# Kernel optimization log

Measured on AMD Instinct MI355X. Metric: run time of the kernel, lower is better.

Reference implementation:

```python
import jax, jax.numpy as jnp
import numpy as np

B, T, E = 4, 2048, 1024
H = 16
QK_SQUEEZE = 2
S = E // QK_SQUEEZE          # squeeze_dim = 512
SHD = S // H                 # squeeze_head_dim = 32
HD = E // H                  # head_dim = 64
SCALING = SHD ** -0.5


def setup_inputs() -> dict:
    key = jax.random.key(0)
    ks = jax.random.split(key, 9)
    def w(k, shape, fan_in):
        return jax.random.normal(k, shape, jnp.float32) * (fan_in ** -0.5)
    return {
        "hidden_states": jax.random.normal(ks[0], (B, T, E), jnp.float32),
        "Wq": w(ks[1], (E, S), E), "bq": jnp.zeros((S,), jnp.float32),
        "Wk": w(ks[2], (E, S), E), "bk": jnp.zeros((S,), jnp.float32),
        "Wv": w(ks[3], (E, E), E), "bv": jnp.zeros((E,), jnp.float32),
        "Wo": w(ks[4], (E, E), E), "bo": jnp.zeros((E,), jnp.float32),
    }


def reference(hidden_states, Wq, bq, Wk, bk, Wv, bv, Wo, bo):
    # Projections; Q pre-scaled as in the torch module.
    q = ((hidden_states @ Wq + bq) * SCALING).reshape(B, T, H, SHD)
    k = (hidden_states @ Wk + bk).reshape(B, T, H, SHD)
    v = (hidden_states @ Wv + bv).reshape(B, T, H, HD)
    # [B, H, Tq, Tk] attention logits with squeezed head dim.
    attn = jnp.einsum("bqhd,bkhd->bhqk", q, k)
    p = jax.nn.softmax(attn, axis=-1)  # dropout p=0.0 -> identity
    out = jnp.einsum("bhqk,bkhd->bqhd", p, v).reshape(B, T, E)
    return out @ Wo + bo
```

## Files before the change

### kernel.cpp

```cpp
#include <hip/hip_runtime.h>
#include <stdint.h>


#define QSCALE (0.17677669529663687f * 1.4426950408889634f)

typedef __bf16 bf16x8 __attribute__((ext_vector_type(8)));
typedef float f32x4 __attribute__((ext_vector_type(4)));
typedef float f32x8 __attribute__((ext_vector_type(8)));
typedef float f32x16 __attribute__((ext_vector_type(16)));
typedef unsigned int u32x2 __attribute__((ext_vector_type(2)));
typedef unsigned int u32x4v __attribute__((ext_vector_type(4)));

static __device__ __forceinline__ unsigned short f2b(float f) {
  return __builtin_bit_cast(unsigned short, (__bf16)f);
}
static __device__ __forceinline__ unsigned int cvtpk(float lo, float hi) {
  unsigned int r;
  asm("v_cvt_pk_bf16_f32 %0, %1, %2" : "=v"(r) : "v"(lo), "v"(hi));
  return r;
}
static __device__ __forceinline__ void gl_lds16(const void* g, void* s) {
  __builtin_amdgcn_global_load_lds(
      (const __attribute__((address_space(1))) unsigned int*)(uintptr_t)g,
      (__attribute__((address_space(3))) unsigned int*)(uintptr_t)s, 16, 0, 0);
}
static __device__ __forceinline__ void pswap(unsigned int& a, unsigned int& b) {
#if __has_builtin(__builtin_amdgcn_permlane32_swap)
  u32x2 r = __builtin_amdgcn_permlane32_swap(a, b, false, false);
  a = r.x;
  b = r.y;
#else
  asm("v_permlane32_swap_b32 %0, %1" : "+v"(a), "+v"(b));
#endif
}

__global__ void k_cvt_hs(const float* __restrict__ in, unsigned short* __restrict__ out) {
  int i = (blockIdx.x * 256 + threadIdx.x) * 4;
  float4 v = *(const float4*)(in + i);
  ushort4 u = make_ushort4(f2b(v.x), f2b(v.y), f2b(v.z), f2b(v.w));
  *(ushort4*)(out + i) = u;
}

__global__ void k_cvt_wT(const float* __restrict__ W, unsigned short* __restrict__ WT,
                         int N, float scale) {
  __shared__ float tile[64][65];
  const int kt = blockIdx.x & 15;
  const int nt = blockIdx.x >> 4;
  const int k0 = kt * 64, n0 = nt * 64;
  const int t = threadIdx.x;
  {
    int kl = t >> 2, c = t & 3;
    const float* src = W + (size_t)(k0 + kl) * N + n0 + c * 16;
#pragma unroll
    for (int j = 0; j < 4; j++) {
      float4 v = *(const float4*)(src + j * 4);
      tile[kl][c * 16 + j * 4 + 0] = v.x;
      tile[kl][c * 16 + j * 4 + 1] = v.y;
      tile[kl][c * 16 + j * 4 + 2] = v.z;
      tile[kl][c * 16 + j * 4 + 3] = v.w;
    }
  }
  __syncthreads();
  {
    int nl = t >> 2, c2 = t & 3;
    unsigned short us[16];
#pragma unroll
    for (int j = 0; j < 16; j++) us[j] = f2b(tile[c2 * 16 + j][nl] * scale);
    uint4 a, b;
    a.x = (unsigned)us[0] | ((unsigned)us[1] << 16);
    a.y = (unsigned)us[2] | ((unsigned)us[3] << 16);
    a.z = (unsigned)us[4] | ((unsigned)us[5] << 16);
    a.w = (unsigned)us[6] | ((unsigned)us[7] << 16);
    b.x = (unsigned)us[8] | ((unsigned)us[9] << 16);
    b.y = (unsigned)us[10] | ((unsigned)us[11] << 16);
    b.z = (unsigned)us[12] | ((unsigned)us[13] << 16);
    b.w = (unsigned)us[14] | ((unsigned)us[15] << 16);
    unsigned short* dst = WT + (size_t)(n0 + nl) * 1024 + k0 + c2 * 16;
    *(uint4*)dst = a;
    *(uint4*)(dst + 8) = b;
  }
}

__global__ void k_bias(const float* __restrict__ bq, const float* __restrict__ bk,
                       const float* __restrict__ bv, float* __restrict__ bqkv) {
  int n = blockIdx.x * 256 + threadIdx.x;
  float v;
  if (n < 512) v = bq[n] * QSCALE;
  else if (n < 1024) v = bk[n - 512];
  else v = bv[n - 1024];
  bqkv[n] = v;
}

template <int MODE>
__global__ __launch_bounds__(256) void k_gemm(
    const unsigned short* __restrict__ A, const unsigned short* __restrict__ BT,
    const float* __restrict__ bias, int M, int N,
    unsigned short* __restrict__ qo, unsigned short* __restrict__ ko,
    unsigned short* __restrict__ vo, float* __restrict__ fo) {
  constexpr int K = 1024;
  __shared__ alignas(128) char smem[16384];
  const int tid = threadIdx.x;
  const int w = tid >> 6, l = tid & 63, lm = l & 15, lc = l >> 4;
  const int nmt = M >> 7;
  const int mt = blockIdx.x % nmt, nt = blockIdx.x / nmt;
  const int brow = mt << 7, bcol = nt << 7;
  const int wm = w >> 1, wn = w & 1;
  f32x4 acc[4][4] = {};
  const int ca = w * 64 + l;

  for (int k0 = 0; k0 < K; k0 += 32) {
#pragma unroll
    for (int j = 0; j < 2; j++) {
      int c = j * 256 + ca;
      gl_lds16(A + (size_t)(brow + (c >> 2)) * K + k0 + (c & 3) * 8,
               smem + (j * 256 + w * 64) * 16);
      gl_lds16(BT + (size_t)(bcol + (c >> 2)) * K + k0 + (c & 3) * 8,
               smem + 8192 + (j * 256 + w * 64) * 16);
    }
    __syncthreads();
    bf16x8 af[4], bf[4];
#pragma unroll
    for (int i = 0; i < 4; i++) {
      af[i] = *(const bf16x8*)(smem + (wm * 64 + i * 16 + lm) * 64 + lc * 16);
      bf[i] = *(const bf16x8*)(smem + 8192 + (wn * 64 + i * 16 + lm) * 64 + lc * 16);
    }
#pragma unroll
    for (int ai = 0; ai < 4; ai++)
#pragma unroll
      for (int bj = 0; bj < 4; bj++)
        acc[ai][bj] = __builtin_amdgcn_mfma_f32_16x16x32_bf16(af[ai], bf[bj], acc[ai][bj], 0, 0, 0);
    __syncthreads();
  }

#pragma unroll
  for (int bj = 0; bj < 4; bj++) {
    const int n = bcol + wn * 64 + bj * 16 + lm;
    const float bv_ = bias[n];
#pragma unroll
    for (int ai = 0; ai < 4; ai++) {
      const int m0 = brow + wm * 64 + ai * 16 + lc * 4;
      f32x4 v = acc[ai][bj];
      const float x0 = v[0] + bv_, x1 = v[1] + bv_, x2 = v[2] + bv_, x3 = v[3] + bv_;
      if constexpr (MODE == 0) {
        const int b = m0 >> 11, t0 = m0 & 2047;
        if (n < 1024) {
          unsigned short* dst = (n < 512) ? qo : ko;
          const int nn = n & 511, h = nn >> 5, d = nn & 31;
          const size_t base = ((size_t)((b << 4) + h) * 2048 + t0) * 32 + d;
          dst[base + 0 * 32] = f2b(x0);
          dst[base + 1 * 32] = f2b(x1);
          dst[base + 2 * 32] = f2b(x2);
          dst[base + 3 * 32] = f2b(x3);
        } else {
          const int e = n - 1024, h = e >> 6, hd = e & 63;
          ushort4 u = make_ushort4(f2b(x0), f2b(x1), f2b(x2), f2b(x3));
          *(ushort4*)(vo + (((size_t)((b << 4) + h) * 256 + (t0 >> 3)) * 64 + hd) * 8 +
                      (t0 & 7)) = u;
        }
      } else {
        float* dst = fo + (size_t)m0 * N + n;
        dst[0 * N] = x0;
        dst[1 * N] = x1;
        dst[2 * N] = x2;
        dst[3 * N] = x3;
      }
    }
  }
}

__global__ __launch_bounds__(128, 2) void k_attn6(
    const unsigned short* __restrict__ qb, const unsigned short* __restrict__ kb,
    const unsigned short* __restrict__ v3, unsigned short* __restrict__ aout) {
  __shared__ float red[64][67];
  const int tid = threadIdx.x, kvh = tid >> 6, l = tid & 63;
  const int l31 = l & 31, hf = l >> 5;
  const int xcd = blockIdx.x & 7, slot = blockIdx.x >> 3;
  const int bh = xcd + ((slot >> 5) << 3);
  const int qrow0 = (slot & 31) << 6;

  const unsigned short* qrow = qb + ((size_t)bh * 2048 + qrow0 + l31) * 32 + hf * 8;
  const bf16x8 qA0 = *(const bf16x8*)(qrow);
  const bf16x8 qA1 = *(const bf16x8*)(qrow + 16);
  const bf16x8 qB0 = *(const bf16x8*)(qrow + 1024);
  const bf16x8 qB1 = *(const bf16x8*)(qrow + 1024 + 16);

  const unsigned short* kp = kb + ((size_t)bh * 2048 + kvh * 1024 + l31) * 32 + hf * 8;
  const unsigned short* vp = v3 + (((size_t)bh * 256 + kvh * 128 + hf) * 64 + l31) * 8;

  f32x16 oA0 = {}, oA1 = {}, oB0 = {}, oB1 = {};
  f32x4 lsA4 = {}, lsB4 = {};

  auto tile_body = [&](bf16x8 kf0, bf16x8 kf1, bf16x8 va00, bf16x8 va01, bf16x8 va10,
                       bf16x8 va11) {
    f32x16 sA = {}, sB = {};
    sA = __builtin_amdgcn_mfma_f32_32x32x16_bf16(kf0, qA0, sA, 0, 0, 0);
    sA = __builtin_amdgcn_mfma_f32_32x32x16_bf16(kf1, qA1, sA, 0, 0, 0);
    sB = __builtin_amdgcn_mfma_f32_32x32x16_bf16(kf0, qB0, sB, 0, 0, 0);
    sB = __builtin_amdgcn_mfma_f32_32x32x16_bf16(kf1, qB1, sB, 0, 0, 0);

#pragma unroll
    for (int i = 0; i < 16; i++) sA[i] = __builtin_amdgcn_exp2f(sA[i]);
#pragma unroll
    for (int i = 0; i < 16; i++) sB[i] = __builtin_amdgcn_exp2f(sB[i]);
    {
      f32x8 t8 = __builtin_shufflevector(sA, sA, 0, 1, 2, 3, 4, 5, 6, 7) +
                 __builtin_shufflevector(sA, sA, 8, 9, 10, 11, 12, 13, 14, 15);
      lsA4 += __builtin_shufflevector(t8, t8, 0, 1, 2, 3) +
              __builtin_shufflevector(t8, t8, 4, 5, 6, 7);
    }
    {
      f32x8 t8 = __builtin_shufflevector(sB, sB, 0, 1, 2, 3, 4, 5, 6, 7) +
                 __builtin_shufflevector(sB, sB, 8, 9, 10, 11, 12, 13, 14, 15);
      lsB4 += __builtin_shufflevector(t8, t8, 0, 1, 2, 3) +
              __builtin_shufflevector(t8, t8, 4, 5, 6, 7);
    }
    unsigned int pa[8], pb[8];
#pragma unroll
    for (int i = 0; i < 8; i++) pa[i] = cvtpk(sA[2 * i], sA[2 * i + 1]);
#pragma unroll
    for (int i = 0; i < 8; i++) pb[i] = cvtpk(sB[2 * i], sB[2 * i + 1]);
    pswap(pa[0], pa[2]);
    pswap(pa[1], pa[3]);
    pswap(pa[4], pa[6]);
    pswap(pa[5], pa[7]);
    pswap(pb[0], pb[2]);
    pswap(pb[1], pb[3]);
    pswap(pb[4], pb[6]);
    pswap(pb[5], pb[7]);
    const bf16x8 fA0 = __builtin_bit_cast(bf16x8, (u32x4v){pa[0], pa[1], pa[2], pa[3]});
    const bf16x8 fA1 = __builtin_bit_cast(bf16x8, (u32x4v){pa[4], pa[5], pa[6], pa[7]});
    const bf16x8 fB0 = __builtin_bit_cast(bf16x8, (u32x4v){pb[0], pb[1], pb[2], pb[3]});
    const bf16x8 fB1 = __builtin_bit_cast(bf16x8, (u32x4v){pb[4], pb[5], pb[6], pb[7]});

    __builtin_amdgcn_s_setprio(1);
    oA0 = __builtin_amdgcn_mfma_f32_32x32x16_bf16(va00, fA0, oA0, 0, 0, 0);
    oA1 = __builtin_amdgcn_mfma_f32_32x32x16_bf16(va01, fA0, oA1, 0, 0, 0);
    oB0 = __builtin_amdgcn_mfma_f32_32x32x16_bf16(va00, fB0, oB0, 0, 0, 0);
    oB1 = __builtin_amdgcn_mfma_f32_32x32x16_bf16(va01, fB0, oB1, 0, 0, 0);
    oA0 = __builtin_amdgcn_mfma_f32_32x32x16_bf16(va10, fA1, oA0, 0, 0, 0);
    oA1 = __builtin_amdgcn_mfma_f32_32x32x16_bf16(va11, fA1, oA1, 0, 0, 0);
    oB0 = __builtin_amdgcn_mfma_f32_32x32x16_bf16(va10, fB1, oB0, 0, 0, 0);
    oB1 = __builtin_amdgcn_mfma_f32_32x32x16_bf16(va11, fB1, oB1, 0, 0, 0);
    __builtin_amdgcn_s_setprio(0);
  };

  bf16x8 kf0 = *(const bf16x8*)(kp);
  bf16x8 kf1 = *(const bf16x8*)(kp + 16);
  bf16x8 va00 = *(const bf16x8*)(vp + 0);
  bf16x8 va01 = *(const bf16x8*)(vp + 256);
  bf16x8 va10 = *(const bf16x8*)(vp + 1024);
  bf16x8 va11 = *(const bf16x8*)(vp + 1280);

  for (int it = 0; it < 31; ++it) {
    kp += 1024;
    vp += 2048;
    const bf16x8 nk0 = *(const bf16x8*)(kp);
    const bf16x8 nk1 = *(const bf16x8*)(kp + 16);
    const bf16x8 nv00 = *(const bf16x8*)(vp + 0);
    const bf16x8 nv01 = *(const bf16x8*)(vp + 256);
    const bf16x8 nv10 = *(const bf16x8*)(vp + 1024);
    const bf16x8 nv11 = *(const bf16x8*)(vp + 1280);

    tile_body(kf0, kf1, va00, va01, va10, va11);

    kf0 = nk0;
    kf1 = nk1;
    va00 = nv00;
    va01 = nv01;
    va10 = nv10;
    va11 = nv11;
  }
  tile_body(kf0, kf1, va00, va01, va10, va11);

  float lsA = (lsA4[0] + lsA4[1]) + (lsA4[2] + lsA4[3]);
  float lsB = (lsB4[0] + lsB4[1]) + (lsB4[2] + lsB4[3]);
  lsA += __shfl_xor(lsA, 32);
  lsB += __shfl_xor(lsB, 32);

  if (kvh == 1) {
    float* r = &red[l][0];
#pragma unroll
    for (int i = 0; i < 16; i++) {
      r[i] = oA0[i];
      r[16 + i] = oA1[i];
      r[32 + i] = oB0[i];
      r[48 + i] = oB1[i];
    }
    r[64] = lsA;
    r[65] = lsB;
  }
  __syncthreads();
  if (kvh == 0) {
    const float* r = &red[l][0];
#pragma unroll
    for (int i = 0; i < 16; i++) {
      oA0[i] += r[i];
      oA1[i] += r[16 + i];
      oB0[i] += r[32 + i];
      oB1[i] += r[48 + i];
    }
    lsA += r[64];
    lsB += r[65];

    const int b = bh >> 4, hh = bh & 15;
    const float rA = 1.0f / lsA, rB = 1.0f / lsB;
    unsigned short* orowA = aout + ((size_t)(b * 2048 + qrow0 + l31)) * 1024 + hh * 64;
    unsigned short* orowB = orowA + (size_t)32 * 1024;
#pragma unroll
    for (int hc = 0; hc < 2; hc++) {
#pragma unroll
      for (int rg = 0; rg < 4; rg++) {
        const f32x16& oa = hc ? oA1 : oA0;
        ushort4 ua = make_ushort4(f2b(oa[rg * 4 + 0] * rA), f2b(oa[rg * 4 + 1] * rA),
                                  f2b(oa[rg * 4 + 2] * rA), f2b(oa[rg * 4 + 3] * rA));
        *(ushort4*)(orowA + hc * 32 + rg * 8 + hf * 4) = ua;
        const f32x16& ob = hc ? oB1 : oB0;
        ushort4 ub = make_ushort4(f2b(ob[rg * 4 + 0] * rB), f2b(ob[rg * 4 + 1] * rB),
                                  f2b(ob[rg * 4 + 2] * rB), f2b(ob[rg * 4 + 3] * rB));
        *(ushort4*)(orowB + hc * 32 + rg * 8 + hf * 4) = ub;
      }
    }
  }
}

extern "C" void kernel_launch(void* const* d_in, const int* in_sizes, int n_in,
                              void* d_out, int out_size, void* d_ws, size_t ws_size,
                              hipStream_t stream) {
  const float* hs = (const float*)d_in[0];
  const float* Wq = (const float*)d_in[1];
  const float* bq = (const float*)d_in[2];
  const float* Wk = (const float*)d_in[3];
  const float* bk = (const float*)d_in[4];
  const float* Wv = (const float*)d_in[5];
  const float* bv = (const float*)d_in[6];
  const float* Wo = (const float*)d_in[7];
  const float* bo = (const float*)d_in[8];

  char* ws = (char*)d_ws;
  unsigned short* hsb   = (unsigned short*)(ws + 0);
  unsigned short* wqkvT = (unsigned short*)(ws + 16777216);
  unsigned short* woT   = (unsigned short*)(ws + 20971520);
  float*          bqkv  = (float*)        (ws + 23068672);
  unsigned short* qbuf  = (unsigned short*)(ws + 23076864);
  unsigned short* kbuf  = (unsigned short*)(ws + 31465472);
  unsigned short* vTb   = (unsigned short*)(ws + 39854080);
  unsigned short* aoutb = (unsigned short*)(ws + 56631296);

  k_cvt_hs<<<8192, 256, 0, stream>>>(hs, hsb);
  k_cvt_wT<<<128, 256, 0, stream>>>(Wq, wqkvT, 512, QSCALE);
  k_cvt_wT<<<128, 256, 0, stream>>>(Wk, wqkvT + 512 * 1024, 512, 1.0f);
  k_cvt_wT<<<256, 256, 0, stream>>>(Wv, wqkvT + 1024 * 1024, 1024, 1.0f);
  k_cvt_wT<<<256, 256, 0, stream>>>(Wo, woT, 1024, 1.0f);
  k_bias<<<8, 256, 0, stream>>>(bq, bk, bv, bqkv);

  k_gemm<0><<<64 * 16, 256, 0, stream>>>(hsb, wqkvT, bqkv, 8192, 2048,
                                         qbuf, kbuf, vTb, nullptr);
  k_attn6<<<2048, 128, 0, stream>>>(qbuf, kbuf, vTb, aoutb);
  k_gemm<1><<<64 * 8, 256, 0, stream>>>(aoutb, woT, bo, 8192, 1024,
                                        nullptr, nullptr, nullptr, (float*)d_out);
}
```

Baseline: 166.9 us.

## Replace QKV projection GEMM with 256x256-tile double-buffered 512-thread kernel

Adds a dedicated QKV GEMM kernel that uses 256x256 output tiles, 512 threads and 128KB of LDS. The K loop is double-buffered, with direct global-to-LDS loads and MFMA phases run at raised wave priority. Larger tiles raise operand reuse per LDS byte, and the 256-block grid covers the GPU in one wave. In exchange, occupancy drops to one block per CU, and the unswizzled 128-byte LDS rows may cause bank conflicts on fragment reads.

```diff
diff --git a/kernel.cpp b/kernel.cpp
--- a/kernel.cpp
+++ b/kernel.cpp
@@ -89,6 +89,109 @@
   else if (n < 1024) v = bk[n - 512];
   else v = bv[n - 1024];
   bqkv[n] = v;
+}
+
+__global__ __launch_bounds__(512, 2) void k_gemm256qkv(
+    const unsigned short* __restrict__ A, const unsigned short* __restrict__ BT,
+    const float* __restrict__ bias,
+    unsigned short* __restrict__ qo, unsigned short* __restrict__ ko,
+    unsigned short* __restrict__ vo) {
+  __shared__ alignas(128) char smem[131072];
+  const int tid = threadIdx.x;
+  const int w = tid >> 6, l = tid & 63, lm = l & 15, lc = l >> 4;
+  const int wm = w >> 2, wn = w & 3;
+  const int mt = blockIdx.x & 31, nt = blockIdx.x >> 5;
+  const int brow = mt << 8, bcol = nt << 8;
+
+  f32x4 acc[8][4] = {};
+
+  auto stage = [&](int kt, int buf) {
+    const unsigned short* As = A + (size_t)brow * 1024 + kt * 64;
+    const unsigned short* Bs = BT + (size_t)bcol * 1024 + kt * 64;
+    char* la = smem + buf * 32768;
+    char* lb = smem + 65536 + buf * 32768;
+#pragma unroll
+    for (int j = 0; j < 4; j++) {
+      const int p = j * 512 + tid;
+      gl_lds16(As + (size_t)(p >> 3) * 1024 + (p & 7) * 8, la + (j * 512 + w * 64) * 16);
+      gl_lds16(Bs + (size_t)(p >> 3) * 1024 + (p & 7) * 8, lb + (j * 512 + w * 64) * 16);
+    }
+  };
+
+  auto phase = [&](const char* la, const char* lb, int mg, int ng) {
+    bf16x8 af[4][2], bf[2][2];
+#pragma unroll
+    for (int mi = 0; mi < 4; mi++)
+#pragma unroll
+      for (int kk = 0; kk < 2; kk++)
+        af[mi][kk] = *(const bf16x8*)(la + (wm * 128 + (mg + mi) * 16 + lm) * 128 +
+                                      kk * 64 + lc * 16);
+#pragma unroll
+    for (int ni = 0; ni < 2; ni++)
+#pragma unroll
+      for (int kk = 0; kk < 2; kk++)
+        bf[ni][kk] = *(const bf16x8*)(lb + (wn * 64 + (ng + ni) * 16 + lm) * 128 +
+                                      kk * 64 + lc * 16);
+    __builtin_amdgcn_s_setprio(1);
+#pragma unroll
+    for (int mi = 0; mi < 4; mi++)
+#pragma unroll
+      for (int ni = 0; ni < 2; ni++)
+#pragma unroll
+        for (int kk = 0; kk < 2; kk++)
+          acc[mg + mi][ng + ni] = __builtin_amdgcn_mfma_f32_16x16x32_bf16(
+              af[mi][kk], bf[ni][kk], acc[mg + mi][ng + ni], 0, 0, 0);
+    __builtin_amdgcn_s_setprio(0);
+    __builtin_amdgcn_sched_barrier(0);
+  };
+
+  auto ktile = [&](int buf) {
+    const char* la = smem + buf * 32768;
+    const char* lb = smem + 65536 + buf * 32768;
+    phase(la, lb, 0, 0);
+    phase(la, lb, 4, 0);
+    phase(la, lb, 0, 2);
+    phase(la, lb, 4, 2);
+  };
+
+  stage(0, 0);
+  __syncthreads();
+#pragma unroll 1
+  for (int kt2 = 0; kt2 < 8; kt2++) {
+    if (kt2 * 2 + 1 < 16) stage(kt2 * 2 + 1, 1);
+    ktile(0);
+    __syncthreads();
+    if (kt2 * 2 + 2 < 16) stage(kt2 * 2 + 2, 0);
+    ktile(1);
+    __syncthreads();
+  }
+
+#pragma unroll
+  for (int nf = 0; nf < 4; nf++) {
+    const int n = bcol + wn * 64 + nf * 16 + lm;
+    const float bv_ = bias[n];
+#pragma unroll
+    for (int mf = 0; mf < 8; mf++) {
+      const int m0 = brow + wm * 128 + mf * 16 + lc * 4;
+      f32x4 v = acc[mf][nf];
+      const float x0 = v[0] + bv_, x1 = v[1] + bv_, x2 = v[2] + bv_, x3 = v[3] + bv_;
+      const int b = m0 >> 11, t0 = m0 & 2047;
+      if (n < 1024) {
+        unsigned short* dst = (n < 512) ? qo : ko;
+        const int nn = n & 511, h = nn >> 5, d = nn & 31;
+        const size_t base = ((size_t)((b << 4) + h) * 2048 + t0) * 32 + d;
+        dst[base + 0 * 32] = f2b(x0);
+        dst[base + 1 * 32] = f2b(x1);
+        dst[base + 2 * 32] = f2b(x2);
+        dst[base + 3 * 32] = f2b(x3);
+      } else {
+        const int e = n - 1024, h = e >> 6, hd = e & 63;
+        ushort4 u = make_ushort4(f2b(x0), f2b(x1), f2b(x2), f2b(x3));
+        *(ushort4*)(vo + (((size_t)((b << 4) + h) * 256 + (t0 >> 3)) * 64 + hd) * 8 +
+                    (t0 & 7)) = u;
+      }
+    }
+  }
 }
 
 template <int MODE>
@@ -353,8 +456,7 @@
   k_cvt_wT<<<256, 256, 0, stream>>>(Wo, woT, 1024, 1.0f);
   k_bias<<<8, 256, 0, stream>>>(bq, bk, bv, bqkv);
 
-  k_gemm<0><<<64 * 16, 256, 0, stream>>>(hsb, wqkvT, bqkv, 8192, 2048,
-                                         qbuf, kbuf, vTb, nullptr);
+  k_gemm256qkv<<<256, 512, 0, stream>>>(hsb, wqkvT, bqkv, qbuf, kbuf, vTb);
   k_attn6<<<2048, 128, 0, stream>>>(qbuf, kbuf, vTb, aoutb);
   k_gemm<1><<<64 * 8, 256, 0, stream>>>(aoutb, woT, bo, 8192, 1024,
                                         nullptr, nullptr, nullptr, (float*)d_out);
```

New measurement: 173.4 us. +3.9%, slower.
